# Kernel optimization log

Measured on AMD Instinct MI355X. Metric: run time of the kernel, lower is better.

The kernel has to match this reference:

```python
import jax, jax.numpy as jnp
import numpy as np

B, T, D, H = 4, 2048, 1024, 16
HD = D // H  # 64


def setup_inputs() -> dict:
    key = jax.random.key(0)
    ks = jax.random.split(key, 5)
    return {
        "x": jax.random.normal(ks[0], (B, T, D), dtype=jnp.float32),
        "W_qkv": jax.random.normal(ks[1], (D, 3 * D), dtype=jnp.float32) * 0.02,
        "b_qkv": jax.random.normal(ks[2], (3 * D,), dtype=jnp.float32) * 0.02,
        "W_out": jax.random.normal(ks[3], (D, D), dtype=jnp.float32) * 0.02,
        "b_out": jax.random.normal(ks[4], (D,), dtype=jnp.float32) * 0.02,
        "mask": 1,
    }


def reference(x, W_qkv, b_qkv, W_out, b_out, mask):
    # fused QKV projection: (B,T,3D)
    qkv = x @ W_qkv + b_qkv
    # torch layout: view (B,T,H,3*hd) then chunk last dim into q,k,v
    qkv = qkv.reshape(B, T, H, 3, HD)
    q = qkv[..., 0, :].transpose(0, 2, 1, 3)  # (B,H,T,hd)
    k = qkv[..., 1, :].transpose(0, 2, 1, 3)
    v = qkv[..., 2, :].transpose(0, 2, 1, 3)
    scores = jnp.einsum('bhqd,bhkd->bhqk', q, k) / jnp.sqrt(jnp.float32(HD))
    if mask:
        causal = jnp.triu(jnp.ones((T, T), dtype=bool), k=1)
        scores = jnp.where(causal[None, None], jnp.float32(-jnp.inf), scores)
    attn = jax.nn.softmax(scores, axis=-1)
    out = jnp.einsum('bhqk,bhkd->bhqd', attn, v)  # (B,H,T,hd)
    out = out.transpose(0, 2, 1, 3).reshape(B, T, D)
    return out @ W_out + b_out
```

## Files before the change

kernel.cpp:

```cpp
#include <hip/hip_runtime.h>

typedef unsigned short u16;
typedef __bf16 bf16x8 __attribute__((ext_vector_type(8)));
typedef float f32x4 __attribute__((ext_vector_type(4)));
typedef float f32x16 __attribute__((ext_vector_type(16)));

#define DEV __device__ __forceinline__

constexpr int Bb = 4, Tt = 2048, Dd = 1024, Hh = 16, HDd = 64;
constexpr int MM = Bb * Tt;
constexpr float QSCALE = 0.125f * 1.4426950408889634f;

DEV u16 f2bf(float f) {
  unsigned u = __float_as_uint(f);
  u += 0x7fffu + ((u >> 16) & 1u);
  return (u16)(u >> 16);
}

DEV unsigned cvtpk(float a, float b) {
  unsigned r;
  asm("v_cvt_pk_bf16_f32 %0, %1, %2" : "=v"(r) : "v"(a), "v"(b));
  return r;
}

DEV void pswap(unsigned& a, unsigned& b) {
  asm("v_permlane32_swap_b32 %0, %1" : "+v"(a), "+v"(b));
}

DEV void gload_lds16(const u16* g, u16* l) {
  __builtin_amdgcn_global_load_lds(
      (const __attribute__((address_space(1))) void*)g,
      (__attribute__((address_space(3))) void*)l, 16, 0, 0);
}

__global__ __launch_bounds__(256) void cast_x_kernel(const float* __restrict__ in,
                                                     u16* __restrict__ out, int n8) {
  int i = blockIdx.x * 256 + threadIdx.x;
  if (i >= n8) return;
  const float4* p = (const float4*)in + (size_t)i * 2;
  float4 v0 = p[0], v1 = p[1];
  union { u16 u[8]; uint4 v; } t;
  t.u[0] = f2bf(v0.x); t.u[1] = f2bf(v0.y); t.u[2] = f2bf(v0.z); t.u[3] = f2bf(v0.w);
  t.u[4] = f2bf(v1.x); t.u[5] = f2bf(v1.y); t.u[6] = f2bf(v1.z); t.u[7] = f2bf(v1.w);
  ((uint4*)out)[i] = t.v;
}

__global__ __launch_bounds__(256) void wcast_t_kernel(const float* __restrict__ in,
                                                      u16* __restrict__ out, int K, int N) {
  __shared__ float tile[32][33];
  int n0 = blockIdx.x * 32, k0 = blockIdx.y * 32;
  int tx = threadIdx.x & 31, ty = threadIdx.x >> 5;
  #pragma unroll
  for (int yy = ty; yy < 32; yy += 8)
    tile[yy][tx] = in[(size_t)(k0 + yy) * N + n0 + tx];
  __syncthreads();
  #pragma unroll
  for (int yy = ty; yy < 32; yy += 8)
    out[(size_t)(n0 + yy) * K + k0 + tx] = f2bf(tile[tx][yy]);
}

DEV void stage256(const u16* __restrict__ src, int row0, int k0, int ld, u16* lds) {
  int t = threadIdx.x;
  #pragma unroll
  for (int j = 0; j < 2; ++j) {
    int e = j * 512 + t;
    int r = e >> 2, slot = e & 3;
    int c = (slot ^ ((r >> 1) & 3)) << 3;
    gload_lds16(src + (size_t)(row0 + r) * ld + k0 + c,
                lds + (size_t)(j * 512 + (t & ~63)) * 8);
  }
}

__global__ __launch_bounds__(512, 2) void gemm256_qkv_kernel(
    const u16* __restrict__ A, const u16* __restrict__ Bt,
    const float* __restrict__ bias,
    u16* __restrict__ Qb, u16* __restrict__ Kb, u16* __restrict__ Vtb,
    int M, int N, int Kd) {
  __shared__ __align__(16) u16 SH[49152];
  int nx = N >> 8;
  int bid = blockIdx.y * nx + blockIdx.x;
  int nwg = (M >> 8) * nx;
  int swz = (bid & 7) * (nwg >> 3) + (bid >> 3);
  int m0 = (swz / nx) * 256, n0 = (swz % nx) * 256;

  int tid = threadIdx.x, l = tid & 63, w = tid >> 6;
  int lq = l & 31, hf = l >> 5;
  int wr = w >> 2, wc = w & 3;
  f32x16 acc[4][2] = {};
  int nk = Kd >> 5;
  stage256(A, m0, 0, Kd, SH);
  stage256(Bt, n0, 0, Kd, SH + 24576);
  stage256(A, m0, 32, Kd, SH + 8192);
  stage256(Bt, n0, 32, Kd, SH + 24576 + 8192);
  asm volatile("s_waitcnt vmcnt(4)" ::: "memory");
  __builtin_amdgcn_s_barrier();
  for (int kt = 0; kt < nk; ++kt) {
    if (kt + 2 < nk) {
      int bi = (kt + 2) % 3;
      stage256(A, m0, (kt + 2) * 32, Kd, SH + bi * 8192);
      stage256(Bt, n0, (kt + 2) * 32, Kd, SH + 24576 + bi * 8192);
    }
    const u16* Ac = SH + (kt % 3) * 8192;
    const u16* Bc = SH + 24576 + (kt % 3) * 8192;
    bf16x8 a[4][2], b[2][2];
    #pragma unroll
    for (int rb = 0; rb < 4; ++rb)
      #pragma unroll
      for (int ks = 0; ks < 2; ++ks) {
        int row = wr * 128 + rb * 32 + lq;
        int s = ks * 2 + hf;
        a[rb][ks] = *(const bf16x8*)&Ac[row * 32 + ((s ^ ((row >> 1) & 3)) << 3)];
      }
    #pragma unroll
    for (int cb = 0; cb < 2; ++cb)
      #pragma unroll
      for (int ks = 0; ks < 2; ++ks) {
        int row = wc * 64 + cb * 32 + lq;
        int s = ks * 2 + hf;
        b[cb][ks] = *(const bf16x8*)&Bc[row * 32 + ((s ^ ((row >> 1) & 3)) << 3)];
      }
    __builtin_amdgcn_s_setprio(1);
    #pragma unroll
    for (int rb = 0; rb < 4; ++rb)
      #pragma unroll
      for (int cb = 0; cb < 2; ++cb)
        #pragma unroll
        for (int ks = 0; ks < 2; ++ks)
          acc[rb][cb] = __builtin_amdgcn_mfma_f32_32x32x16_bf16(
              a[rb][ks], b[cb][ks], acc[rb][cb], 0, 0, 0);
    __builtin_amdgcn_s_setprio(0);
    if (kt + 2 < nk) {
      asm volatile("s_waitcnt vmcnt(4)" ::: "memory");
    } else {
      asm volatile("s_waitcnt vmcnt(0)" ::: "memory");
    }
    __builtin_amdgcn_s_barrier();
  }
  u16* ep = SH + w * 4096;
  int nblk = n0 + wc * 64;
  int hh = nblk / 192, seg = (nblk % 192) >> 6;
  int mbase = m0 + wr * 128;
  int b_ = mbase >> 11;
  float bv0 = bias[nblk + lq];
  float bv1 = bias[nblk + 32 + lq];
  if (seg == 2) {
    u16* dst0 = Vtb + (size_t)(b_ * Hh + hh) * HDd * Tt;
    #pragma unroll
    for (int rh = 0; rh < 2; ++rh) {
      #pragma unroll
      for (int cb = 0; cb < 2; ++cb) {
        float bv = cb ? bv1 : bv0;
        int prow = cb * 32 + lq;
        #pragma unroll
        for (int rr = 0; rr < 2; ++rr) {
          int rb = 2 * rh + rr;
          #pragma unroll
          for (int g16 = 0; g16 < 16; ++g16) {
            int pcol = rr * 32 + (g16 & 3) + 8 * (g16 >> 2) + 4 * hf;
            int slot = pcol >> 3;
            ep[prow * 64 + ((slot ^ (prow & 7)) << 3) + (pcol & 7)] =
                f2bf(acc[rb][cb][g16] + bv);
          }
        }
      }
      asm volatile("s_waitcnt lgkmcnt(0)" ::: "memory");
      int t0 = (mbase + rh * 64) & (Tt - 1);
      #pragma unroll
      for (int s = 0; s < 8; ++s) {
        int row = s * 8 + (l >> 3);
        int phys = ((l & 7) ^ (row & 7)) << 3;
        uint4 v = *(const uint4*)&ep[row * 64 + phys];
        *(uint4*)(dst0 + (size_t)row * Tt + t0 + (l & 7) * 8) = v;
      }
      asm volatile("s_waitcnt lgkmcnt(0)" ::: "memory");
    }
  } else {
    float qs = (seg == 0) ? QSCALE : 1.0f;
    u16* dstbase = ((seg == 0) ? Qb : Kb) + (size_t)(b_ * Hh + hh) * Tt * HDd;
    #pragma unroll
    for (int rh = 0; rh < 2; ++rh) {
      #pragma unroll
      for (int rr = 0; rr < 2; ++rr) {
        int rb = 2 * rh + rr;
        #pragma unroll
        for (int cb = 0; cb < 2; ++cb) {
          float bv = cb ? bv1 : bv0;
          int pcol = cb * 32 + lq;
          int slot = pcol >> 3;
          #pragma unroll
          for (int g16 = 0; g16 < 16; ++g16) {
            int prow = rr * 32 + (g16 & 3) + 8 * (g16 >> 2) + 4 * hf;
            ep[prow * 64 + ((slot ^ (prow & 7)) << 3) + (pcol & 7)] =
                f2bf((acc[rb][cb][g16] + bv) * qs);
          }
        }
      }
      asm volatile("s_waitcnt lgkmcnt(0)" ::: "memory");
      int t0 = (mbase + rh * 64) & (Tt - 1);
      u16* dst = dstbase + (size_t)t0 * HDd;
      #pragma unroll
      for (int s = 0; s < 8; ++s) {
        int row = s * 8 + (l >> 3);
        int phys = ((l & 7) ^ (row & 7)) << 3;
        uint4 v = *(const uint4*)&ep[row * 64 + phys];
        *(uint4*)(dst + row * 64 + (l & 7) * 8) = v;
      }
      asm volatile("s_waitcnt lgkmcnt(0)" ::: "memory");
    }
  }
}

DEV void stage_tile(const u16* __restrict__ src, int row0, int k0, int ld, u16* lds) {
  int t = threadIdx.x, w = t >> 6;
  #pragma unroll
  for (int j = 0; j < 2; ++j) {
    int e = (j * 256 + t) * 8;
    int r = e >> 5;
    int slot = (e >> 3) & 3;
    int c = (slot ^ ((r >> 1) & 3)) << 3;
    gload_lds16(src + (size_t)(row0 + r) * ld + k0 + c, lds + j * 2048 + w * 512);
  }
}

__global__ __launch_bounds__(256) void gemm_out_kernel(
    const u16* __restrict__ A, const u16* __restrict__ Bt,
    const float* __restrict__ bias, float* __restrict__ Cf,
    int M, int N, int Kd) {
  __shared__ __align__(16) u16 SH[24576];
  int nx = N >> 7;
  int bid = blockIdx.y * nx + blockIdx.x;
  int nwg = (M >> 7) * nx;
  int swz = (bid & 7) * (nwg >> 3) + (bid >> 3);
  int m0 = (swz / nx) * 128, n0 = (swz % nx) * 128;

  int tid = threadIdx.x, l = tid & 63, w = tid >> 6;
  int lo = l & 15, g = l >> 4;
  int wm = (w >> 1) * 64, wn = (w & 1) * 64;
  f32x4 acc[4][4] = {};
  int nk = Kd >> 5;
  stage_tile(A, m0, 0, Kd, SH);
  stage_tile(Bt, n0, 0, Kd, SH + 12288);
  stage_tile(A, m0, 32, Kd, SH + 4096);
  stage_tile(Bt, n0, 32, Kd, SH + 12288 + 4096);
  asm volatile("s_waitcnt vmcnt(4)" ::: "memory");
  __builtin_amdgcn_s_barrier();
  for (int kt = 0; kt < nk; ++kt) {
    if (kt + 2 < nk) {
      int bi = (kt + 2) % 3;
      stage_tile(A, m0, (kt + 2) * 32, Kd, SH + bi * 4096);
      stage_tile(Bt, n0, (kt + 2) * 32, Kd, SH + 12288 + bi * 4096);
    }
    const u16* Ac = SH + (kt % 3) * 4096;
    const u16* Bc = SH + 12288 + (kt % 3) * 4096;
    bf16x8 a[4], b[4];
    #pragma unroll
    for (int i = 0; i < 4; ++i) {
      int row = wm + i * 16 + lo;
      a[i] = *(const bf16x8*)&Ac[row * 32 + ((g ^ ((row >> 1) & 3)) << 3)];
    }
    #pragma unroll
    for (int j = 0; j < 4; ++j) {
      int row = wn + j * 16 + lo;
      b[j] = *(const bf16x8*)&Bc[row * 32 + ((g ^ ((row >> 1) & 3)) << 3)];
    }
    #pragma unroll
    for (int i = 0; i < 4; ++i)
      #pragma unroll
      for (int j = 0; j < 4; ++j)
        acc[i][j] = __builtin_amdgcn_mfma_f32_16x16x32_bf16(a[i], b[j], acc[i][j], 0, 0, 0);
    if (kt + 2 < nk) {
      asm volatile("s_waitcnt vmcnt(4)" ::: "memory");
    } else {
      asm volatile("s_waitcnt vmcnt(0)" ::: "memory");
    }
    __builtin_amdgcn_s_barrier();
  }
  #pragma unroll
  for (int j = 0; j < 4; ++j) {
    int n = n0 + wn + j * 16 + lo;
    float bv = bias[n];
    #pragma unroll
    for (int i = 0; i < 4; ++i) {
      #pragma unroll
      for (int r = 0; r < 4; ++r) {
        int m = m0 + wm + i * 16 + g * 4 + r;
        Cf[(size_t)m * N + n] = acc[i][j][r] + bv;
      }
    }
  }
}

DEV void stage512(const u16* __restrict__ g, size_t rstride, u16* lds) {
  int t = threadIdx.x;
  int r = t >> 3, pp = t & 7;
  int lg = pp ^ (r & 7);
  gload_lds16(g + (size_t)r * rstride + lg * 8, lds + (size_t)(t & ~63) * 8);
}

DEV void build_pfrags(const f32x16& s, bf16x8& f0, bf16x8& f1) {
  unsigned w0 = cvtpk(s[0], s[1]),  w1 = cvtpk(s[2], s[3]);
  unsigned w2 = cvtpk(s[4], s[5]),  w3 = cvtpk(s[6], s[7]);
  unsigned w4 = cvtpk(s[8], s[9]),  w5 = cvtpk(s[10], s[11]);
  unsigned w6 = cvtpk(s[12], s[13]), w7 = cvtpk(s[14], s[15]);
  pswap(w0, w2);
  pswap(w1, w3);
  pswap(w4, w6);
  pswap(w5, w7);
  union { unsigned u[4]; bf16x8 v; } t0, t1;
  t0.u[0] = w0; t0.u[1] = w1; t0.u[2] = w2; t0.u[3] = w3;
  t1.u[0] = w4; t1.u[1] = w5; t1.u[2] = w6; t1.u[3] = w7;
  f0 = t0.v; f1 = t1.v;
}

DEV void write_o(u16* __restrict__ O, size_t rowbase, const f32x16& o0,
                 const f32x16& o1, float L, int hf) {
  float inv = 1.0f / L;
  #pragma unroll
  for (int m = 0; m < 4; ++m) {
    uint2 v0, v1;
    v0.x = cvtpk(o0[4 * m] * inv,     o0[4 * m + 1] * inv);
    v0.y = cvtpk(o0[4 * m + 2] * inv, o0[4 * m + 3] * inv);
    *(uint2*)(O + rowbase + m * 8 + hf * 4) = v0;
    v1.x = cvtpk(o1[4 * m] * inv,     o1[4 * m + 1] * inv);
    v1.y = cvtpk(o1[4 * m + 2] * inv, o1[4 * m + 3] * inv);
    *(uint2*)(O + rowbase + 32 + m * 8 + hf * 4) = v1;
  }
}

__global__ __launch_bounds__(512) void attn_kernel(const u16* __restrict__ Q,
                                                   const u16* __restrict__ K,
                                                   const u16* __restrict__ Vt,
                                                   u16* __restrict__ O) {
  __shared__ __align__(16) u16 Ks[4][4096];
  __shared__ __align__(16) u16 Vs[4][4096];
  __shared__ float MLs[8][64][2];
  __shared__ float OSs[4][64][8];
  int p = blockIdx.y & 7;
  int bh = ((int)blockIdx.y >> 3) * 8 + (int)blockIdx.x;
  int b_ = bh >> 4, h = bh & 15;
  const u16* Qp = Q + (size_t)bh * Tt * HDd;
  const u16* Kp = K + (size_t)bh * Tt * HDd;
  const u16* Vp = Vt + (size_t)bh * HDd * Tt;
  int tid = threadIdx.x, w = tid >> 6, l = tid & 63;
  int wq = w & 3, grp = w >> 2;
  int lq = l & 31, hf = l >> 5;
  int JA = 15 - p, JB = p;
  int ntA = 2 * JA + 2;
  constexpr int ntT = 34;

  int q0 = 128 * JA + 32 * wq;
  int qrow = q0 + lq;
  int swz = lq & 7;

  bf16x8 aq[4];
  #pragma unroll
  for (int s = 0; s < 4; ++s)
    aq[s] = *(const bf16x8*)(Qp + (size_t)qrow * HDd + s * 16 + hf * 8);

  f32x16 o0 = {}, o1 = {};
  float M = -1e30f, L = 0.f;

  stage512(Kp, HDd, Ks[0]);
  stage512(Vp, Tt, Vs[0]);
  stage512(Kp + (size_t)64 * HDd, HDd, Ks[1]);
  stage512(Vp + 64, Tt, Vs[1]);
  asm volatile("s_waitcnt vmcnt(0)" ::: "memory");
  __builtin_amdgcn_s_barrier();

  int jB = ntA >> 1;
  for (int j = 0; j < ntT / 2; ++j) {
    int t2 = 2 * j + 2;
    if (t2 < ntT) {
      int kt2 = (t2 < ntA ? t2 : t2 - ntA) * 64;
      stage512(Kp + (size_t)kt2 * HDd, HDd, Ks[t2 & 3]);
      stage512(Vp + kt2, Tt, Vs[t2 & 3]);
      int t3 = t2 + 1;
      int kt3 = (t3 < ntA ? t3 : t3 - ntA) * 64;
      stage512(Kp + (size_t)kt3 * HDd, HDd, Ks[t3 & 3]);
      stage512(Vp + kt3, Tt, Vs[t3 & 3]);
    }
    if (j == jB) {
      MLs[w][l][0] = M; MLs[w][l][1] = L;
      asm volatile("s_waitcnt lgkmcnt(0)" ::: "memory");
      __builtin_amdgcn_s_barrier();
      float Mb = MLs[w ^ 4][l][0], Lb = MLs[w ^ 4][l][1];
      float Mstar = fmaxf(M, Mb);
      float ss = __builtin_amdgcn_exp2f(M - Mstar);
      float sb = __builtin_amdgcn_exp2f(Mb - Mstar);
      float Lm = L * ss + Lb * sb;
      #pragma unroll
      for (int r = 0; r < 16; ++r) { o0[r] *= ss; o1[r] *= ss; }
      #pragma unroll
      for (int c = 0; c < 4; ++c) {
        if (w >= 4) {
          #pragma unroll
          for (int k = 0; k < 8; ++k)
            OSs[wq][l][k] = (c < 2) ? o0[(c & 1) * 8 + k] : o1[(c & 1) * 8 + k];
        }
        asm volatile("s_waitcnt lgkmcnt(0)" ::: "memory");
        __builtin_amdgcn_s_barrier();
        if (w < 4) {
          #pragma unroll
          for (int k = 0; k < 8; ++k) {
            float v = OSs[wq][l][k];
            if (c < 2) o0[(c & 1) * 8 + k] += v; else o1[(c & 1) * 8 + k] += v;
          }
        }
        asm volatile("s_waitcnt lgkmcnt(0)" ::: "memory");
        __builtin_amdgcn_s_barrier();
      }
      if (w < 4) {
        size_t rbA = ((size_t)b_ * Tt + qrow) * Dd + h * HDd;
        write_o(O, rbA, o0, o1, Lm, hf);
      }
      #pragma unroll
      for (int r = 0; r < 16; ++r) { o0[r] = 0.f; o1[r] = 0.f; }
      M = -1e30f; L = 0.f;
      q0 = 128 * JB + 32 * wq;
      qrow = q0 + lq;
      #pragma unroll
      for (int s = 0; s < 4; ++s)
        aq[s] = *(const bf16x8*)(Qp + (size_t)qrow * HDd + s * 16 + hf * 8);
    }
    int myt = 2 * j + grp;
    int kt = (myt < ntA ? myt : myt - ntA) * 64;
    const u16* Kc = Ks[myt & 3];
    const u16* Vc = Vs[myt & 3];
    if (kt < q0 + 32) {
      f32x16 s0 = {}, s1 = {};
      __builtin_amdgcn_s_setprio(1);
      #pragma unroll
      for (int ds = 0; ds < 4; ++ds) {
        int slot = 2 * ds + hf;
        bf16x8 k0 = *(const bf16x8*)&Kc[lq * 64 + ((slot ^ swz) << 3)];
        bf16x8 k1 = *(const bf16x8*)&Kc[(32 + lq) * 64 + ((slot ^ swz) << 3)];
        s0 = __builtin_amdgcn_mfma_f32_32x32x16_bf16(k0, aq[ds], s0, 0, 0, 0);
        s1 = __builtin_amdgcn_mfma_f32_32x32x16_bf16(k1, aq[ds], s1, 0, 0, 0);
      }
      __builtin_amdgcn_s_setprio(0);
      if (kt + 63 > q0) {
        #pragma unroll
        for (int r = 0; r < 16; ++r) {
          int kg = kt + (r & 3) + 8 * (r >> 2) + 4 * hf;
          if (kg > qrow)      s0[r] = -INFINITY;
          if (kg + 32 > qrow) s1[r] = -INFINITY;
        }
      }
      float mx_[16];
      #pragma unroll
      for (int r = 0; r < 16; ++r) mx_[r] = fmaxf(s0[r], s1[r]);
      #pragma unroll
      for (int st = 8; st >= 1; st >>= 1)
        #pragma unroll
        for (int r = 0; r < 16; ++r) if (r < st) mx_[r] = fmaxf(mx_[r], mx_[r + st]);
      float mx = fmaxf(mx_[0], __shfl_xor(mx_[0], 32));
      float sc = 1.f;
      if (!__all(mx <= M + 8.f)) {
        float Mn = fmaxf(M, mx);
        sc = __builtin_amdgcn_exp2f(M - Mn);
        M = Mn;
        #pragma unroll
        for (int r = 0; r < 16; ++r) { o0[r] *= sc; o1[r] *= sc; }
      }
      #pragma unroll
      for (int r = 0; r < 16; ++r) {
        s0[r] = __builtin_amdgcn_exp2f(s0[r] - M);
        s1[r] = __builtin_amdgcn_exp2f(s1[r] - M);
      }
      float ls_[16];
      #pragma unroll
      for (int r = 0; r < 16; ++r) ls_[r] = s0[r] + s1[r];
      #pragma unroll
      for (int st = 8; st >= 1; st >>= 1)
        #pragma unroll
        for (int r = 0; r < 16; ++r) if (r < st) ls_[r] += ls_[r + st];
      float ls = ls_[0] + __shfl_xor(ls_[0], 32);
      L = L * sc + ls;
      bf16x8 pf0, pf1, pf2, pf3;
      build_pfrags(s0, pf0, pf1);
      build_pfrags(s1, pf2, pf3);
      __builtin_amdgcn_s_setprio(1);
      #pragma unroll
      for (int ks = 0; ks < 4; ++ks) {
        int slot = 2 * ks + hf;
        bf16x8 v0 = *(const bf16x8*)&Vc[lq * 64 + ((slot ^ swz) << 3)];
        bf16x8 v1 = *(const bf16x8*)&Vc[(32 + lq) * 64 + ((slot ^ swz) << 3)];
        bf16x8 pf = (ks == 0) ? pf0 : (ks == 1) ? pf1 : (ks == 2) ? pf2 : pf3;
        o0 = __builtin_amdgcn_mfma_f32_32x32x16_bf16(v0, pf, o0, 0, 0, 0);
        o1 = __builtin_amdgcn_mfma_f32_32x32x16_bf16(v1, pf, o1, 0, 0, 0);
      }
      __builtin_amdgcn_s_setprio(0);
    }
    asm volatile("s_waitcnt vmcnt(0)" ::: "memory");
    __builtin_amdgcn_s_barrier();
  }

  MLs[w][l][0] = M; MLs[w][l][1] = L;
  asm volatile("s_waitcnt lgkmcnt(0)" ::: "memory");
  __builtin_amdgcn_s_barrier();
  float Mb = MLs[w ^ 4][l][0], Lb = MLs[w ^ 4][l][1];
  float Mstar = fmaxf(M, Mb);
  float ss = __builtin_amdgcn_exp2f(M - Mstar);
  float sb = __builtin_amdgcn_exp2f(Mb - Mstar);
  float Lm = L * ss + Lb * sb;
  #pragma unroll
  for (int r = 0; r < 16; ++r) { o0[r] *= ss; o1[r] *= ss; }
  #pragma unroll
  for (int c = 0; c < 4; ++c) {
    if (w >= 4) {
      #pragma unroll
      for (int k = 0; k < 8; ++k)
        OSs[wq][l][k] = (c < 2) ? o0[(c & 1) * 8 + k] : o1[(c & 1) * 8 + k];
    }
    asm volatile("s_waitcnt lgkmcnt(0)" ::: "memory");
    __builtin_amdgcn_s_barrier();
    if (w < 4) {
      #pragma unroll
      for (int k = 0; k < 8; ++k) {
        float v = OSs[wq][l][k];
        if (c < 2) o0[(c & 1) * 8 + k] += v; else o1[(c & 1) * 8 + k] += v;
      }
    }
    asm volatile("s_waitcnt lgkmcnt(0)" ::: "memory");
    __builtin_amdgcn_s_barrier();
  }
  if (w < 4) {
    size_t rbB = ((size_t)b_ * Tt + qrow) * Dd + h * HDd;
    write_o(O, rbB, o0, o1, Lm, hf);
  }
}

extern "C" void kernel_launch(void* const* d_in, const int* in_sizes, int n_in,
                              void* d_out, int out_size, void* d_ws, size_t ws_size,
                              hipStream_t stream) {
  const float* x    = (const float*)d_in[0];
  const float* Wqkv = (const float*)d_in[1];
  const float* bqkv = (const float*)d_in[2];
  const float* Wout = (const float*)d_in[3];
  const float* bout = (const float*)d_in[4];
  float* out = (float*)d_out;
  char* ws = (char*)d_ws;

  u16* xb    = (u16*)(ws + 0);
  u16* Ob    = (u16*)(ws + 0);
  u16* Wqkvt = (u16*)(ws + 16777216);
  u16* Woutt = (u16*)(ws + 23068672);
  u16* Qb    = (u16*)(ws + 25165824);
  u16* Kb    = (u16*)(ws + 41943040);
  u16* Vtb   = (u16*)(ws + 58720256);

  cast_x_kernel<<<4096, 256, 0, stream>>>(x, xb, (MM * Dd) / 8);
  wcast_t_kernel<<<dim3(96, 32), 256, 0, stream>>>(Wqkv, Wqkvt, Dd, 3 * Dd);
  wcast_t_kernel<<<dim3(32, 32), 256, 0, stream>>>(Wout, Woutt, Dd, Dd);
  gemm256_qkv_kernel<<<dim3(12, 32), 512, 0, stream>>>(
      xb, Wqkvt, bqkv, Qb, Kb, Vtb, MM, 3 * Dd, Dd);
  attn_kernel<<<dim3(8, 64), 512, 0, stream>>>(Qb, Kb, Vtb, Ob);
  gemm_out_kernel<<<dim3(8, 64), 256, 0, stream>>>(
      Ob, Woutt, bout, out, MM, Dd, Dd);
}
```

Before: 185.7 us.

## Switch QKV GEMM to 16x16x32 MFMA with double-buffered LDS staging

Replaces the 32x32x16 MFMA tiling in the QKV projection GEMM with a 16x16x32 MFMA tiling (8x4 accumulator fragments per wave). It also cuts the three-stage LDS prefetch ring to two-stage double buffering, which shrinks shared memory from 96KB to 64KB. The epilogue is rewritten to match the new accumulator layout. The smaller LDS footprint may help occupancy, but the shallower pipeline waits on vmcnt(0) every iteration, which can expose global load latency. The new layout also issues more LDS reads per MFMA.

```diff
diff --git a/kernel.cpp b/kernel.cpp
--- a/kernel.cpp
+++ b/kernel.cpp
@@ -76,7 +76,7 @@
     const float* __restrict__ bias,
     u16* __restrict__ Qb, u16* __restrict__ Kb, u16* __restrict__ Vtb,
     int M, int N, int Kd) {
-  __shared__ __align__(16) u16 SH[49152];
+  __shared__ __align__(16) u16 SH[32768];
   int nx = N >> 8;
   int bid = blockIdx.y * nx + blockIdx.x;
   int nwg = (M >> 8) * nx;
@@ -84,82 +84,66 @@
   int m0 = (swz / nx) * 256, n0 = (swz % nx) * 256;
 
   int tid = threadIdx.x, l = tid & 63, w = tid >> 6;
-  int lq = l & 31, hf = l >> 5;
+  int lo = l & 15, g = l >> 4;
   int wr = w >> 2, wc = w & 3;
-  f32x16 acc[4][2] = {};
+  int wm = wr * 128, wn = wc * 64;
+  f32x4 acc[8][4] = {};
   int nk = Kd >> 5;
   stage256(A, m0, 0, Kd, SH);
-  stage256(Bt, n0, 0, Kd, SH + 24576);
-  stage256(A, m0, 32, Kd, SH + 8192);
-  stage256(Bt, n0, 32, Kd, SH + 24576 + 8192);
-  asm volatile("s_waitcnt vmcnt(4)" ::: "memory");
+  stage256(Bt, n0, 0, Kd, SH + 16384);
+  asm volatile("s_waitcnt vmcnt(0)" ::: "memory");
   __builtin_amdgcn_s_barrier();
   for (int kt = 0; kt < nk; ++kt) {
-    if (kt + 2 < nk) {
-      int bi = (kt + 2) % 3;
-      stage256(A, m0, (kt + 2) * 32, Kd, SH + bi * 8192);
-      stage256(Bt, n0, (kt + 2) * 32, Kd, SH + 24576 + bi * 8192);
-    }
-    const u16* Ac = SH + (kt % 3) * 8192;
-    const u16* Bc = SH + 24576 + (kt % 3) * 8192;
-    bf16x8 a[4][2], b[2][2];
-    #pragma unroll
-    for (int rb = 0; rb < 4; ++rb)
-      #pragma unroll
-      for (int ks = 0; ks < 2; ++ks) {
-        int row = wr * 128 + rb * 32 + lq;
-        int s = ks * 2 + hf;
-        a[rb][ks] = *(const bf16x8*)&Ac[row * 32 + ((s ^ ((row >> 1) & 3)) << 3)];
-      }
-    #pragma unroll
-    for (int cb = 0; cb < 2; ++cb)
-      #pragma unroll
-      for (int ks = 0; ks < 2; ++ks) {
-        int row = wc * 64 + cb * 32 + lq;
-        int s = ks * 2 + hf;
-        b[cb][ks] = *(const bf16x8*)&Bc[row * 32 + ((s ^ ((row >> 1) & 3)) << 3)];
-      }
+    int cur = kt & 1;
+    if (kt + 1 < nk) {
+      stage256(A, m0, (kt + 1) * 32, Kd, SH + (cur ^ 1) * 8192);
+      stage256(Bt, n0, (kt + 1) * 32, Kd, SH + 16384 + (cur ^ 1) * 8192);
+    }
+    const u16* Ac = SH + cur * 8192;
+    const u16* Bc = SH + 16384 + cur * 8192;
+    bf16x8 a[8], b[4];
+    #pragma unroll
+    for (int i = 0; i < 8; ++i) {
+      int row = wm + i * 16 + lo;
+      a[i] = *(const bf16x8*)&Ac[row * 32 + ((g ^ ((row >> 1) & 3)) << 3)];
+    }
+    #pragma unroll
+    for (int j = 0; j < 4; ++j) {
+      int row = wn + j * 16 + lo;
+      b[j] = *(const bf16x8*)&Bc[row * 32 + ((g ^ ((row >> 1) & 3)) << 3)];
+    }
     __builtin_amdgcn_s_setprio(1);
     #pragma unroll
-    for (int rb = 0; rb < 4; ++rb)
-      #pragma unroll
-      for (int cb = 0; cb < 2; ++cb)
-        #pragma unroll
-        for (int ks = 0; ks < 2; ++ks)
-          acc[rb][cb] = __builtin_amdgcn_mfma_f32_32x32x16_bf16(
-              a[rb][ks], b[cb][ks], acc[rb][cb], 0, 0, 0);
+    for (int i = 0; i < 8; ++i)
+      #pragma unroll
+      for (int j = 0; j < 4; ++j)
+        acc[i][j] = __builtin_amdgcn_mfma_f32_16x16x32_bf16(a[i], b[j], acc[i][j], 0, 0, 0);
     __builtin_amdgcn_s_setprio(0);
-    if (kt + 2 < nk) {
-      asm volatile("s_waitcnt vmcnt(4)" ::: "memory");
-    } else {
-      asm volatile("s_waitcnt vmcnt(0)" ::: "memory");
-    }
+    asm volatile("s_waitcnt vmcnt(0)" ::: "memory");
     __builtin_amdgcn_s_barrier();
   }
   u16* ep = SH + w * 4096;
-  int nblk = n0 + wc * 64;
+  int nblk = n0 + wn;
   int hh = nblk / 192, seg = (nblk % 192) >> 6;
-  int mbase = m0 + wr * 128;
+  int mbase = m0 + wm;
   int b_ = mbase >> 11;
-  float bv0 = bias[nblk + lq];
-  float bv1 = bias[nblk + 32 + lq];
   if (seg == 2) {
     u16* dst0 = Vtb + (size_t)(b_ * Hh + hh) * HDd * Tt;
     #pragma unroll
     for (int rh = 0; rh < 2; ++rh) {
       #pragma unroll
-      for (int cb = 0; cb < 2; ++cb) {
-        float bv = cb ? bv1 : bv0;
-        int prow = cb * 32 + lq;
+      for (int j = 0; j < 4; ++j) {
+        float bv = bias[nblk + j * 16 + lo];
+        int prow = j * 16 + lo;
         #pragma unroll
-        for (int rr = 0; rr < 2; ++rr) {
-          int rb = 2 * rh + rr;
+        for (int ii = 0; ii < 4; ++ii) {
+          int i = rh * 4 + ii;
           #pragma unroll
-          for (int g16 = 0; g16 < 16; ++g16) {
-            int pcol = rr * 32 + (g16 & 3) + 8 * (g16 >> 2) + 4 * hf;
+          for (int r = 0; r < 4; ++r) {
+            int pcol = ii * 16 + g * 4 + r;
             int slot = pcol >> 3;
             ep[prow * 64 + ((slot ^ (prow & 7)) << 3) + (pcol & 7)] =
-                f2bf(acc[rb][cb][g16] + bv);
+                f2bf(acc[i][j][r] + bv);
           }
         }
       }
@@ -180,18 +164,17 @@
     #pragma unroll
     for (int rh = 0; rh < 2; ++rh) {
       #pragma unroll
-      for (int rr = 0; rr < 2; ++rr) {
-        int rb = 2 * rh + rr;
+      for (int j = 0; j < 4; ++j) {
+        float bv = bias[nblk + j * 16 + lo];
+        int slot = j * 2 + (lo >> 3);
         #pragma unroll
-        for (int cb = 0; cb < 2; ++cb) {
-          float bv = cb ? bv1 : bv0;
-          int pcol = cb * 32 + lq;
-          int slot = pcol >> 3;
+        for (int ii = 0; ii < 4; ++ii) {
+          int i = rh * 4 + ii;
           #pragma unroll
-          for (int g16 = 0; g16 < 16; ++g16) {
-            int prow = rr * 32 + (g16 & 3) + 8 * (g16 >> 2) + 4 * hf;
-            ep[prow * 64 + ((slot ^ (prow & 7)) << 3) + (pcol & 7)] =
-                f2bf((acc[rb][cb][g16] + bv) * qs);
+          for (int r = 0; r < 4; ++r) {
+            int lrow = ii * 16 + g * 4 + r;
+            ep[lrow * 64 + ((slot ^ (lrow & 7)) << 3) + (lo & 7)] =
+                f2bf((acc[i][j][r] + bv) * qs);
           }
         }
       }
```

After: 180.3 us. 2.9% less time.
